# Kernel optimization log

Measured on AMD Instinct MI355X. Metric: run time of the kernel, lower is better.

The kernel has to match this reference:

```python
import jax, jax.numpy as jnp
import numpy as np

B, S, H = 2, 2048, 1024
NH, HD = 16, 64            # num heads, head dim
R = 8                      # lora rank
LORA_SCALE = 64.0 / 8.0    # lora_alpha / lora_rank
SCALE = jnp.sqrt(jnp.float32(HD))


def setup_inputs() -> dict:
    key = jax.random.key(0)
    ks = jax.random.split(key, 14)
    std = 1.0 / np.sqrt(H)
    p = {
        'hidden_states': jax.random.normal(ks[0], (B, S, H), jnp.float32),
        'attention_mask': jnp.ones((B, S), jnp.float32),
        # base projections, stored [in, out] so y = x @ W
        'Wq': jax.random.normal(ks[1], (H, H), jnp.float32) * std,
        'Wk': jax.random.normal(ks[2], (H, H), jnp.float32) * std,
        'Wv': jax.random.normal(ks[3], (H, H), jnp.float32) * std,
        'Wo': jax.random.normal(ks[4], (H, H), jnp.float32) * std,
        # LoRA down (A: [H,R]) / up (B: [R,H]) for q,k,v,output
        'Aq': jax.random.normal(ks[5], (H, R), jnp.float32) * 0.01,
        'Bq': jax.random.normal(ks[6], (R, H), jnp.float32) * 0.01,
        'Ak': jax.random.normal(ks[7], (H, R), jnp.float32) * 0.01,
        'Bk': jax.random.normal(ks[8], (R, H), jnp.float32) * 0.01,
        'Av': jax.random.normal(ks[9], (H, R), jnp.float32) * 0.01,
        'Bv': jax.random.normal(ks[10], (R, H), jnp.float32) * 0.01,
        'Ao': jax.random.normal(ks[11], (H, R), jnp.float32) * 0.01,
        'Bo': jax.random.normal(ks[12], (R, H), jnp.float32) * 0.01,
    }
    return p


def _heads(x):
    # [B,S,H] -> [B,NH,S,HD]
    return x.reshape(B, S, NH, HD).transpose(0, 2, 1, 3)


def reference(hidden_states, attention_mask, Wq, Wk, Wv, Wo,
              Aq, Bq, Ak, Bk, Av, Bv, Ao, Bo):
    hs = hidden_states
    sg = jax.lax.stop_gradient  # freeze_base=True: base projections are no_grad

    q = sg(hs @ Wq) + (hs @ Aq) @ Bq * LORA_SCALE
    k = sg(hs @ Wk) + (hs @ Ak) @ Bk * LORA_SCALE
    v = sg(hs @ Wv) + (hs @ Av) @ Bv * LORA_SCALE

    qh, kh, vh = _heads(q), _heads(k), _heads(v)  # [B,NH,S,HD]

    scores = jnp.einsum('bhqd,bhkd->bhqk', qh, kh) / SCALE  # [B,NH,S,S]
    mask = (1.0 - attention_mask)[:, None, None, :] * -10000.0
    scores = scores + mask
    probs = jax.nn.softmax(scores, axis=-1)  # dropout is identity in eval

    ctx = jnp.einsum('bhqk,bhkd->bhqd', probs, vh)
    ctx = ctx.transpose(0, 2, 1, 3).reshape(B, S, H)

    out = sg(ctx @ Wo) + (ctx @ Ao) @ Bo * LORA_SCALE
    return out
```

## Files before the change

### kernel.cpp

```cpp
#include <hip/hip_runtime.h>
#include <math.h>

typedef float fx4 __attribute__((ext_vector_type(4)));
typedef float f32x4 __attribute__((ext_vector_type(4)));
typedef short bf16x8 __attribute__((ext_vector_type(8)));
typedef unsigned short us4 __attribute__((ext_vector_type(4)));
typedef unsigned short us8 __attribute__((ext_vector_type(8)));
typedef unsigned int u32x4 __attribute__((ext_vector_type(4)));

#define HDIM 1024
#define SEQ  2048
#define BATCH 2
#define NHEAD 16
#define HD    64
#define MTOT  4096
#define LSCALE 8.0f
#define LOG2E 1.44269504088896340736f

__device__ __forceinline__ unsigned short f2bf(float f) {
    union { float f; unsigned int u; } v; v.f = f;
    unsigned int r = v.u + 0x7FFFu + ((v.u >> 16) & 1u);
    return (unsigned short)(r >> 16);
}
__device__ __forceinline__ float bf2f(unsigned short h) {
    union { unsigned int u; float f; } v; v.u = ((unsigned int)h) << 16;
    return v.f;
}
__device__ __forceinline__ unsigned int cvt_pk_bf16(float a, float b) {
    unsigned int r;
    asm("v_cvt_pk_bf16_f32 %0, %1, %2" : "=v"(r) : "v"(a), "v"(b));
    return r;
}

__global__ __launch_bounds__(256)
void split_x_kernel(const float* __restrict__ X, unsigned short* __restrict__ Xh,
                    unsigned short* __restrict__ Xl, int n4)
{
    int i = blockIdx.x * 256 + threadIdx.x;
    int stride = gridDim.x * 256;
    for (; i < n4; i += stride) {
        fx4 v = *((const fx4*)X + i);
        us4 h, l;
#pragma unroll
        for (int j = 0; j < 4; ++j) {
            h[j] = f2bf(v[j]);
            l[j] = f2bf(v[j] - bf2f(h[j]));
        }
        *((us4*)Xh + i) = h;
        *((us4*)Xl + i) = l;
    }
}

__global__ __launch_bounds__(256)
void tsplit_w_kernel(const float* __restrict__ W0, const float* __restrict__ W1,
                     const float* __restrict__ W2, const float* __restrict__ W3,
                     unsigned short* __restrict__ WTbase)
{
    int z = blockIdx.z;
    const float* W = (z == 0) ? W0 : (z == 1) ? W1 : (z == 2) ? W2 : W3;
    unsigned short* WTh = WTbase + (size_t)z * 2097152;
    unsigned short* WTl = WTh + 1048576;
    int n0 = blockIdx.x * 64, k0 = blockIdx.y * 64;
    __shared__ unsigned int T[64][65];
    int t = threadIdx.x;
#pragma unroll
    for (int i = 0; i < 4; ++i) {
        int idx = t + 256 * i;
        int r = idx >> 4, c4 = (idx & 15) * 4;
        fx4 w = *(const fx4*)&W[(size_t)(k0 + r) * HDIM + n0 + c4];
#pragma unroll
        for (int j = 0; j < 4; ++j) {
            unsigned short hi = f2bf(w[j]);
            unsigned short lo = f2bf(w[j] - bf2f(hi));
            T[r][c4 + j] = (unsigned int)hi | ((unsigned int)lo << 16);
        }
    }
    __syncthreads();
#pragma unroll
    for (int i = 0; i < 4; ++i) {
        int idx = t + 256 * i;
        int n = idx >> 4, kg = (idx & 15) * 4;
        us4 hv, lv;
#pragma unroll
        for (int j = 0; j < 4; ++j) {
            unsigned int p = T[kg + j][n];
            hv[j] = (unsigned short)(p & 0xffffu);
            lv[j] = (unsigned short)(p >> 16);
        }
        *(us4*)&WTh[(size_t)(n0 + n) * HDIM + k0 + kg] = hv;
        *(us4*)&WTl[(size_t)(n0 + n) * HDIM + k0 + kg] = lv;
    }
}

__global__ __launch_bounds__(256)
void transpose_v_kernel(const unsigned short* __restrict__ vb,
                        unsigned short* __restrict__ vt)
{
    int s0 = blockIdx.x * 64;
    int bh = blockIdx.y;
    int b = bh >> 4, h = bh & 15;
    __shared__ unsigned short T[64][80];
    int t = threadIdx.x;
#pragma unroll
    for (int i = 0; i < 2; ++i) {
        int u = t + 256 * i;
        int r = u >> 3, cg = u & 7;
        us8 v = *(const us8*)&vb[(size_t)(b * SEQ + s0 + r) * HDIM + h * HD + 8 * cg];
        *(us8*)&T[r][8 * cg] = v;
    }
    __syncthreads();
#pragma unroll
    for (int i = 0; i < 2; ++i) {
        int u = t + 256 * i;
        int d = u & 63, sg = u >> 6;
        us8 v;
#pragma unroll
        for (int j = 0; j < 8; ++j) v[j] = T[8 * sg + j][d];
        *(us8*)&vt[(size_t)(bh * HD + d) * SEQ + s0 + 8 * sg] = v;
    }
}

__global__ __launch_bounds__(64)
void lora_down_kernel(const float* __restrict__ X,
                      const float* __restrict__ A0,
                      const float* __restrict__ A1,
                      const float* __restrict__ A2,
                      float* __restrict__ out, int nmat)
{
    int row  = blockIdx.x;
    int lane = threadIdx.x;
    const float* xr = X + (size_t)row * HDIM;
    float xv[16];
#pragma unroll
    for (int i = 0; i < 16; ++i) xv[i] = xr[lane + 64 * i];
    const float* Amats[3] = {A0, A1, A2};
    for (int m = 0; m < nmat; ++m) {
        const float* A = Amats[m];
        float s[8];
#pragma unroll
        for (int c = 0; c < 8; ++c) s[c] = 0.f;
#pragma unroll
        for (int i = 0; i < 16; ++i) {
            const float* ap = A + (size_t)(lane + 64 * i) * 8;
#pragma unroll
            for (int c = 0; c < 8; ++c) s[c] += xv[i] * ap[c];
        }
#pragma unroll
        for (int c = 0; c < 8; ++c) {
#pragma unroll
            for (int off = 1; off < 64; off <<= 1)
                s[c] += __shfl_xor(s[c], off, 64);
        }
        if (lane == 0) {
#pragma unroll
            for (int c = 0; c < 8; ++c)
                out[(size_t)row * 24 + m * 8 + c] = s[c];
        }
    }
}

__global__ __launch_bounds__(64)
void lora_down_bf_kernel(const unsigned short* __restrict__ Xh,
                         const unsigned short* __restrict__ Xl,
                         const float* __restrict__ A,
                         float* __restrict__ out)
{
    int row  = blockIdx.x;
    int lane = threadIdx.x;
    const unsigned short* xh = Xh + (size_t)row * HDIM;
    const unsigned short* xl = Xl + (size_t)row * HDIM;
    float xv[16];
#pragma unroll
    for (int i = 0; i < 16; ++i)
        xv[i] = bf2f(xh[lane + 64 * i]) + bf2f(xl[lane + 64 * i]);
    float s[8];
#pragma unroll
    for (int c = 0; c < 8; ++c) s[c] = 0.f;
#pragma unroll
    for (int i = 0; i < 16; ++i) {
        const float* ap = A + (size_t)(lane + 64 * i) * 8;
#pragma unroll
        for (int c = 0; c < 8; ++c) s[c] += xv[i] * ap[c];
    }
#pragma unroll
    for (int c = 0; c < 8; ++c) {
#pragma unroll
        for (int off = 1; off < 64; off <<= 1)
            s[c] += __shfl_xor(s[c], off, 64);
    }
    if (lane == 0) {
#pragma unroll
        for (int c = 0; c < 8; ++c) out[(size_t)row * 8 + c] = s[c];
    }
}

template<bool OUTF32, int BM>
__global__ __launch_bounds__(256, BM == 128 ? 2 : 3)
void gemm_mfma_kernel(const unsigned short* __restrict__ Xh, const unsigned short* __restrict__ Xl,
                      const unsigned short* __restrict__ WTbase, int wsel0,
                      const float* __restrict__ XA, int xa_stride, int xa_off0,
                      const float* __restrict__ Bu0, const float* __restrict__ Bu1, const float* __restrict__ Bu2,
                      void* __restrict__ O0, void* __restrict__ O1, void* __restrict__ O2)
{
    constexpr int FN = (BM == 128) ? 4 : 2;
    int pz = blockIdx.z;
    const unsigned short* WTh = WTbase + (size_t)(wsel0 + pz) * 2097152;
    const unsigned short* WTl = WTh + 1048576;
    const float* Bu = (pz == 0) ? Bu0 : (pz == 1) ? Bu1 : Bu2;
    void* Ovp       = (pz == 0) ? O0 : (pz == 1) ? O1 : O2;
    int xa_off = xa_off0 + pz * 8;

    int brow = blockIdx.y * BM, bcol = blockIdx.x * 128;
    int t = threadIdx.x, wid = t >> 6, lane = t & 63, l15 = lane & 15, g = lane >> 4;
    int wm = (BM == 128) ? (wid >> 1) * 64 : 0;
    int wn = (BM == 128) ? (wid & 1) * 64 : wid * 32;

    __shared__ unsigned short Ah[BM][40];
    __shared__ unsigned short Al[BM][40];
    __shared__ unsigned short Bh[128][40];
    __shared__ unsigned short Bl[128][40];

    f32x4 acc[4][FN];
#pragma unroll
    for (int i = 0; i < 4; ++i)
#pragma unroll
        for (int j = 0; j < FN; ++j) acc[i][j] = (f32x4){0.f, 0.f, 0.f, 0.f};

    int sm = t >> 2, skg = t & 3;
    const unsigned short* aH0 = Xh  + (size_t)(brow + sm) * HDIM + 8 * skg;
    const unsigned short* aL0 = Xl  + (size_t)(brow + sm) * HDIM + 8 * skg;
    const unsigned short* bH0 = WTh + (size_t)(bcol + sm) * HDIM + 8 * skg;
    const unsigned short* bL0 = WTl + (size_t)(bcol + sm) * HDIM + 8 * skg;
    const size_t R64 = (size_t)64 * HDIM;

    us8 rAH0, rAH1, rAL0, rAL1, rBH0, rBH1, rBL0, rBL1;
    rAH0 = *(const us8*)(aH0);
    rAL0 = *(const us8*)(aL0);
    if (BM == 128) {
        rAH1 = *(const us8*)(aH0 + R64);
        rAL1 = *(const us8*)(aL0 + R64);
    }
    rBH0 = *(const us8*)(bH0);
    rBH1 = *(const us8*)(bH0 + R64);
    rBL0 = *(const us8*)(bL0);
    rBL1 = *(const us8*)(bL0 + R64);

    for (int k0 = 0; k0 < HDIM; k0 += 32) {
        __syncthreads();
        *(us8*)&Ah[sm][8 * skg] = rAH0;
        *(us8*)&Al[sm][8 * skg] = rAL0;
        if (BM == 128) {
            *(us8*)&Ah[(sm + 64) & (BM - 1)][8 * skg] = rAH1;
            *(us8*)&Al[(sm + 64) & (BM - 1)][8 * skg] = rAL1;
        }
        *(us8*)&Bh[sm][8 * skg]      = rBH0;
        *(us8*)&Bh[sm + 64][8 * skg] = rBH1;
        *(us8*)&Bl[sm][8 * skg]      = rBL0;
        *(us8*)&Bl[sm + 64][8 * skg] = rBL1;
        __syncthreads();
        if (k0 + 32 < HDIM) {
            int ko = k0 + 32;
            rAH0 = *(const us8*)(aH0 + ko);
            rAL0 = *(const us8*)(aL0 + ko);
            if (BM == 128) {
                rAH1 = *(const us8*)(aH0 + R64 + ko);
                rAL1 = *(const us8*)(aL0 + R64 + ko);
            }
            rBH0 = *(const us8*)(bH0 + ko);
            rBH1 = *(const us8*)(bH0 + R64 + ko);
            rBL0 = *(const us8*)(bL0 + ko);
            rBL1 = *(const us8*)(bL0 + R64 + ko);
        }
        bf16x8 fah[4], fal[4], fbh[FN], fbl[FN];
#pragma unroll
        for (int f = 0; f < 4; ++f) {
            fah[f] = *(const bf16x8*)&Ah[wm + 16 * f + l15][8 * g];
            fal[f] = *(const bf16x8*)&Al[wm + 16 * f + l15][8 * g];
        }
#pragma unroll
        for (int f = 0; f < FN; ++f) {
            fbh[f] = *(const bf16x8*)&Bh[wn + 16 * f + l15][8 * g];
            fbl[f] = *(const bf16x8*)&Bl[wn + 16 * f + l15][8 * g];
        }
#pragma unroll
        for (int fm = 0; fm < 4; ++fm)
#pragma unroll
            for (int fn = 0; fn < FN; ++fn) {
                f32x4 a = acc[fm][fn];
                a = __builtin_amdgcn_mfma_f32_16x16x32_bf16(fah[fm], fbh[fn], a, 0, 0, 0);
                a = __builtin_amdgcn_mfma_f32_16x16x32_bf16(fah[fm], fbl[fn], a, 0, 0, 0);
                a = __builtin_amdgcn_mfma_f32_16x16x32_bf16(fal[fm], fbh[fn], a, 0, 0, 0);
                acc[fm][fn] = a;
            }
    }

    float lb[8][FN];
#pragma unroll
    for (int rr = 0; rr < 8; ++rr)
#pragma unroll
        for (int fn = 0; fn < FN; ++fn)
            lb[rr][fn] = Bu[(size_t)rr * HDIM + bcol + wn + 16 * fn + l15] * LSCALE;

#pragma unroll
    for (int fm = 0; fm < 4; ++fm) {
        float la[4][8];
#pragma unroll
        for (int r = 0; r < 4; ++r) {
            int row = brow + wm + 16 * fm + 4 * g + r;
            const float* lap = XA + (size_t)row * xa_stride + xa_off;
            fx4 q0 = *(const fx4*)lap;
            fx4 q1 = *(const fx4*)(lap + 4);
#pragma unroll
            for (int j = 0; j < 4; ++j) { la[r][j] = q0[j]; la[r][4 + j] = q1[j]; }
        }
#pragma unroll
        for (int fn = 0; fn < FN; ++fn)
#pragma unroll
            for (int r = 0; r < 4; ++r) {
                float sum = acc[fm][fn][r];
#pragma unroll
                for (int rr = 0; rr < 8; ++rr) sum += la[r][rr] * lb[rr][fn];
                size_t row = (size_t)(brow + wm + 16 * fm + 4 * g + r);
                int col = bcol + wn + 16 * fn + l15;
                if (OUTF32) ((float*)Ovp)[row * HDIM + col] = sum;
                else ((unsigned short*)Ovp)[row * HDIM + col] = f2bf(sum);
            }
    }
}

#define QBLK 64
#define KVB  64
#define NT   (SEQ / KVB)

__global__ __launch_bounds__(256, 4)
void attn_mfma_kernel(const unsigned short* __restrict__ Qg, const unsigned short* __restrict__ Kg,
                      const unsigned short* __restrict__ Vt, const float* __restrict__ mask,
                      unsigned short* __restrict__ Ch, unsigned short* __restrict__ Cl)
{
    int qt = blockIdx.x, h = blockIdx.y, b = blockIdx.z;
    int t    = threadIdx.x;
    int wid  = t >> 6;
    int lane = t & 63;
    int l15  = lane & 15;
    int g    = lane >> 4;

    __shared__ __align__(16) unsigned short Ks[2][64][72];
    __shared__ __align__(16) unsigned short Vs[2][64][72];
    __shared__ __align__(16) float Msd[2][64];

    bf16x8 qa[2];
    const unsigned short* qp = Qg + (size_t)(b * SEQ + qt * QBLK + wid * 16) * HDIM + h * HD;
#pragma unroll
    for (int kc = 0; kc < 2; ++kc)
        qa[kc] = *(const bf16x8*)(qp + (size_t)l15 * HDIM + 32 * kc + 8 * g);

    float m0 = 0.f;
    f32x4 l4 = (f32x4){0.f, 0.f, 0.f, 0.f};
    f32x4 acc[4];
#pragma unroll
    for (int n = 0; n < 4; ++n) acc[n] = (f32x4){0.f, 0.f, 0.f, 0.f};

    const unsigned short* kp0 = Kg + (size_t)(b * SEQ) * HDIM + h * HD;
    const unsigned short* vt0 = Vt + (size_t)((b * NHEAD + h) * HD) * SEQ;

    const float QSCL = 0.125f * LOG2E;
    const float MSCL = -10000.0f * LOG2E;

    int r0 = t >> 3,           c0 = (t & 7) * 8;
    int r1 = (t + 256) >> 3,   c1 = c0;

    *(us8*)&Ks[0][r0][c0] = *(const us8*)(kp0 + (size_t)r0 * HDIM + c0);
    *(us8*)&Ks[0][r1][c1] = *(const us8*)(kp0 + (size_t)r1 * HDIM + c1);
    *(us8*)&Vs[0][r0][c0] = *(const us8*)(vt0 + (size_t)r0 * SEQ + c0);
    *(us8*)&Vs[0][r1][c1] = *(const us8*)(vt0 + (size_t)r1 * SEQ + c1);
    if (t < 64) Msd[0][t] = (1.0f - mask[b * SEQ + t]) * MSCL;
    __syncthreads();

    int cur = 0;
    for (int kt = 0; kt < NT; ++kt) {
        us8 knr0, knr1, vnr0, vnr1;
        float mreg = 1.0f;
        bool more = (kt + 1 < NT);
        if (more) {
            const unsigned short* kp = kp0 + (size_t)(kt + 1) * KVB * HDIM;
            const unsigned short* vp = vt0 + (kt + 1) * KVB;
            knr0 = *(const us8*)(kp + (size_t)r0 * HDIM + c0);
            knr1 = *(const us8*)(kp + (size_t)r1 * HDIM + c1);
            vnr0 = *(const us8*)(vp + (size_t)r0 * SEQ + c0);
            vnr1 = *(const us8*)(vp + (size_t)r1 * SEQ + c1);
            if (t < 64) mreg = mask[b * SEQ + (kt + 1) * KVB + t];
        }

        f32x4 sT[4];
#pragma unroll
        for (int n = 0; n < 4; ++n) {
            f32x4 a = (f32x4){0.f, 0.f, 0.f, 0.f};
#pragma unroll
            for (int kc = 0; kc < 2; ++kc) {
                bf16x8 kb = *(const bf16x8*)&Ks[cur][16 * n + l15][32 * kc + 8 * g];
                a = __builtin_amdgcn_mfma_f32_16x16x32_bf16(kb, qa[kc], a, 0, 0, 0);
            }
            sT[n] = a;
        }

#pragma unroll
        for (int n = 0; n < 4; ++n) {
            fx4 msk = *(const fx4*)&Msd[cur][16 * n + 4 * g];
#pragma unroll
            for (int r = 0; r < 4; ++r) sT[n][r] = fmaf(sT[n][r], QSCL, msk[r]);
        }

        if (kt == 0) {
            f32x4 t01, t23, tt;
#pragma unroll
            for (int r = 0; r < 4; ++r) {
                t01[r] = fmaxf(sT[0][r], sT[1][r]);
                t23[r] = fmaxf(sT[2][r], sT[3][r]);
                tt[r]  = fmaxf(t01[r], t23[r]);
            }
            float mx = fmaxf(fmaxf(tt[0], tt[1]), fmaxf(tt[2], tt[3]));
            mx = fmaxf(mx, __shfl_xor(mx, 16, 64));
            mx = fmaxf(mx, __shfl_xor(mx, 32, 64));
            m0 = fmaxf(mx, -64.f);
        }

#pragma unroll
        for (int n = 0; n < 4; ++n)
#pragma unroll
            for (int r = 0; r < 4; ++r) {
                float p = exp2f(sT[n][r] - m0);
                sT[n][r] = p;
                l4[r] += p;
            }

        unsigned int pkx[4], pky[4];
#pragma unroll
        for (int n = 0; n < 4; ++n) {
            pkx[n] = cvt_pk_bf16(sT[n][0], sT[n][1]);
            pky[n] = cvt_pk_bf16(sT[n][2], sT[n][3]);
        }

        int lA = l15 + 32 * (g & 1);
        int lB = lA + 16;
        bool selhi = (g & 2) != 0;
        bf16x8 pb[2];
#pragma unroll
        for (int kc = 0; kc < 2; ++kc) {
            unsigned int xA0 = __shfl((int)pkx[2 * kc], lA, 64);
            unsigned int yA0 = __shfl((int)pky[2 * kc], lA, 64);
            unsigned int xA1 = __shfl((int)pkx[2 * kc + 1], lA, 64);
            unsigned int yA1 = __shfl((int)pky[2 * kc + 1], lA, 64);
            unsigned int xB0 = __shfl((int)pkx[2 * kc], lB, 64);
            unsigned int yB0 = __shfl((int)pky[2 * kc], lB, 64);
            unsigned int xB1 = __shfl((int)pkx[2 * kc + 1], lB, 64);
            unsigned int yB1 = __shfl((int)pky[2 * kc + 1], lB, 64);
            u32x4 d;
            d[0] = selhi ? xA1 : xA0;
            d[1] = selhi ? yA1 : yA0;
            d[2] = selhi ? xB1 : xB0;
            d[3] = selhi ? yB1 : yB0;
            pb[kc] = *(bf16x8*)&d;
        }

#pragma unroll
        for (int n = 0; n < 4; ++n)
#pragma unroll
            for (int kc = 0; kc < 2; ++kc) {
                bf16x8 vb = *(const bf16x8*)&Vs[cur][16 * n + l15][32 * kc + 8 * g];
                acc[n] = __builtin_amdgcn_mfma_f32_16x16x32_bf16(vb, pb[kc], acc[n], 0, 0, 0);
            }

        if (more) {
            *(us8*)&Ks[cur ^ 1][r0][c0] = knr0;
            *(us8*)&Ks[cur ^ 1][r1][c1] = knr1;
            *(us8*)&Vs[cur ^ 1][r0][c0] = vnr0;
            *(us8*)&Vs[cur ^ 1][r1][c1] = vnr1;
            if (t < 64) Msd[cur ^ 1][t] = (1.0f - mreg) * MSCL;
        }
        __syncthreads();
        cur ^= 1;
    }

    float l = (l4[0] + l4[1]) + (l4[2] + l4[3]);
    l += __shfl_xor(l, 16, 64);
    l += __shfl_xor(l, 32, 64);
    float inv = 1.0f / l;
    size_t row = (size_t)(b * SEQ + qt * QBLK + wid * 16 + l15);
#pragma unroll
    for (int n = 0; n < 4; ++n) {
        us4 hv, lv;
#pragma unroll
        for (int r = 0; r < 4; ++r) {
            float o = acc[n][r] * inv;
            unsigned short hi = f2bf(o);
            hv[r] = hi;
            lv[r] = f2bf(o - bf2f(hi));
        }
        size_t idx = row * HDIM + h * HD + 16 * n + 4 * g;
        *(us4*)&Ch[idx] = hv;
        *(us4*)&Cl[idx] = lv;
    }
}

extern "C" void kernel_launch(void* const* d_in, const int* in_sizes, int n_in,
                              void* d_out, int out_size, void* d_ws, size_t ws_size,
                              hipStream_t stream)
{
    const float* hs   = (const float*)d_in[0];
    const float* mask = (const float*)d_in[1];
    const float* Wq = (const float*)d_in[2];
    const float* Wk = (const float*)d_in[3];
    const float* Wv = (const float*)d_in[4];
    const float* Wo = (const float*)d_in[5];
    const float* Aq = (const float*)d_in[6];
    const float* Bq = (const float*)d_in[7];
    const float* Ak = (const float*)d_in[8];
    const float* Bk = (const float*)d_in[9];
    const float* Av = (const float*)d_in[10];
    const float* Bv = (const float*)d_in[11];
    const float* Ao = (const float*)d_in[12];
    const float* Bo = (const float*)d_in[13];
    float* out = (float*)d_out;

    char* w = (char*)d_ws;
    unsigned short* Xh = (unsigned short*)(w);
    unsigned short* Xl = (unsigned short*)(w + ((size_t)8 << 20));
    unsigned short* WT = (unsigned short*)(w + ((size_t)16 << 20));
    unsigned short* qb = (unsigned short*)(w + ((size_t)32 << 20));
    unsigned short* kb = (unsigned short*)(w + ((size_t)40 << 20));
    unsigned short* vb = (unsigned short*)(w + ((size_t)48 << 20));
    unsigned short* vt = (unsigned short*)(w + ((size_t)56 << 20));
    float* hsA  = (float*)(w + ((size_t)64 << 20));
    float* ctxA = (float*)(w + ((size_t)64 << 20) + 400 * 1024);

    split_x_kernel<<<2048, 256, 0, stream>>>(hs, Xh, Xl, MTOT * HDIM / 4);
    tsplit_w_kernel<<<dim3(16, 16, 4), 256, 0, stream>>>(Wq, Wk, Wv, Wo, WT);
    lora_down_kernel<<<MTOT, 64, 0, stream>>>(hs, Aq, Ak, Av, hsA, 3);
    gemm_mfma_kernel<false, 128><<<dim3(8, 32, 3), 256, 0, stream>>>(
        Xh, Xl, WT, 0, hsA, 24, 0, Bq, Bk, Bv, qb, kb, vb);
    transpose_v_kernel<<<dim3(SEQ / 64, BATCH * NHEAD), 256, 0, stream>>>(vb, vt);
    attn_mfma_kernel<<<dim3(SEQ / QBLK, NHEAD, BATCH), 256, 0, stream>>>(
        qb, kb, vt, mask, Xh , Xl );
    lora_down_bf_kernel<<<MTOT, 64, 0, stream>>>(Xh, Xl, Ao, ctxA);
    gemm_mfma_kernel<true, 64><<<dim3(8, 64, 1), 256, 0, stream>>>(
        Xh, Xl, WT, 3, ctxA, 8, 0, Bo, Bo, Bo, out, out, out);
}
```

Before: 245.4 us.

## Process two query subtiles per wave in attention to reuse K/V fragments

Doubles the query block to 128 rows, with each wave computing two 16-row subtiles against the same K and V LDS fragments. This halves LDS reads and global K/V loads per query and gives more independent MFMAs per loaded fragment. In exchange it uses more registers, lowers the launch-bounds occupancy target and halves the number of blocks, which reduces parallelism and latency hiding.

After: 240.1 us. -2.2%, faster.

```diff
diff --git a/kernel.cpp b/kernel.cpp
--- a/kernel.cpp
+++ b/kernel.cpp
@@ -328,11 +328,11 @@
     }
 }
 
-#define QBLK 64
+#define QBLK 128
 #define KVB  64
 #define NT   (SEQ / KVB)
 
-__global__ __launch_bounds__(256, 4)
+__global__ __launch_bounds__(256, 2)
 void attn_mfma_kernel(const unsigned short* __restrict__ Qg, const unsigned short* __restrict__ Kg,
                       const unsigned short* __restrict__ Vt, const float* __restrict__ mask,
                       unsigned short* __restrict__ Ch, unsigned short* __restrict__ Cl)
@@ -348,17 +348,23 @@
     __shared__ __align__(16) unsigned short Vs[2][64][72];
     __shared__ __align__(16) float Msd[2][64];
 
-    bf16x8 qa[2];
-    const unsigned short* qp = Qg + (size_t)(b * SEQ + qt * QBLK + wid * 16) * HDIM + h * HD;
-#pragma unroll
-    for (int kc = 0; kc < 2; ++kc)
-        qa[kc] = *(const bf16x8*)(qp + (size_t)l15 * HDIM + 32 * kc + 8 * g);
-
-    float m0 = 0.f;
-    f32x4 l4 = (f32x4){0.f, 0.f, 0.f, 0.f};
-    f32x4 acc[4];
-#pragma unroll
-    for (int n = 0; n < 4; ++n) acc[n] = (f32x4){0.f, 0.f, 0.f, 0.f};
+    bf16x8 qa[2][2];
+    const unsigned short* qp = Qg + (size_t)(b * SEQ + qt * QBLK + wid * 32) * HDIM + h * HD;
+#pragma unroll
+    for (int m = 0; m < 2; ++m)
+#pragma unroll
+        for (int kc = 0; kc < 2; ++kc)
+            qa[m][kc] = *(const bf16x8*)(qp + (size_t)(16 * m + l15) * HDIM + 32 * kc + 8 * g);
+
+    float m0[2] = {0.f, 0.f};
+    f32x4 l4[2];
+    f32x4 acc[2][4];
+#pragma unroll
+    for (int m = 0; m < 2; ++m) {
+        l4[m] = (f32x4){0.f, 0.f, 0.f, 0.f};
+#pragma unroll
+        for (int n = 0; n < 4; ++n) acc[m][n] = (f32x4){0.f, 0.f, 0.f, 0.f};
+    }
 
     const unsigned short* kp0 = Kg + (size_t)(b * SEQ) * HDIM + h * HD;
     const unsigned short* vt0 = Vt + (size_t)((b * NHEAD + h) * HD) * SEQ;
@@ -391,84 +397,97 @@
             if (t < 64) mreg = mask[b * SEQ + (kt + 1) * KVB + t];
         }
 
-        f32x4 sT[4];
+        f32x4 sT[2][4];
 #pragma unroll
         for (int n = 0; n < 4; ++n) {
-            f32x4 a = (f32x4){0.f, 0.f, 0.f, 0.f};
-#pragma unroll
-            for (int kc = 0; kc < 2; ++kc) {
-                bf16x8 kb = *(const bf16x8*)&Ks[cur][16 * n + l15][32 * kc + 8 * g];
-                a = __builtin_amdgcn_mfma_f32_16x16x32_bf16(kb, qa[kc], a, 0, 0, 0);
-            }
-            sT[n] = a;
+            bf16x8 kb0 = *(const bf16x8*)&Ks[cur][16 * n + l15][8 * g];
+            bf16x8 kb1 = *(const bf16x8*)&Ks[cur][16 * n + l15][32 + 8 * g];
+#pragma unroll
+            for (int m = 0; m < 2; ++m) {
+                f32x4 a = (f32x4){0.f, 0.f, 0.f, 0.f};
+                a = __builtin_amdgcn_mfma_f32_16x16x32_bf16(kb0, qa[m][0], a, 0, 0, 0);
+                a = __builtin_amdgcn_mfma_f32_16x16x32_bf16(kb1, qa[m][1], a, 0, 0, 0);
+                sT[m][n] = a;
+            }
         }
 
 #pragma unroll
         for (int n = 0; n < 4; ++n) {
             fx4 msk = *(const fx4*)&Msd[cur][16 * n + 4 * g];
 #pragma unroll
-            for (int r = 0; r < 4; ++r) sT[n][r] = fmaf(sT[n][r], QSCL, msk[r]);
+            for (int m = 0; m < 2; ++m)
+#pragma unroll
+                for (int r = 0; r < 4; ++r) sT[m][n][r] = fmaf(sT[m][n][r], QSCL, msk[r]);
         }
 
         if (kt == 0) {
-            f32x4 t01, t23, tt;
-#pragma unroll
-            for (int r = 0; r < 4; ++r) {
-                t01[r] = fmaxf(sT[0][r], sT[1][r]);
-                t23[r] = fmaxf(sT[2][r], sT[3][r]);
-                tt[r]  = fmaxf(t01[r], t23[r]);
-            }
-            float mx = fmaxf(fmaxf(tt[0], tt[1]), fmaxf(tt[2], tt[3]));
-            mx = fmaxf(mx, __shfl_xor(mx, 16, 64));
-            mx = fmaxf(mx, __shfl_xor(mx, 32, 64));
-            m0 = fmaxf(mx, -64.f);
-        }
-
-#pragma unroll
-        for (int n = 0; n < 4; ++n)
-#pragma unroll
-            for (int r = 0; r < 4; ++r) {
-                float p = exp2f(sT[n][r] - m0);
-                sT[n][r] = p;
-                l4[r] += p;
-            }
-
-        unsigned int pkx[4], pky[4];
-#pragma unroll
-        for (int n = 0; n < 4; ++n) {
-            pkx[n] = cvt_pk_bf16(sT[n][0], sT[n][1]);
-            pky[n] = cvt_pk_bf16(sT[n][2], sT[n][3]);
-        }
+#pragma unroll
+            for (int m = 0; m < 2; ++m) {
+                f32x4 tt;
+#pragma unroll
+                for (int r = 0; r < 4; ++r)
+                    tt[r] = fmaxf(fmaxf(sT[m][0][r], sT[m][1][r]), fmaxf(sT[m][2][r], sT[m][3][r]));
+                float mx = fmaxf(fmaxf(tt[0], tt[1]), fmaxf(tt[2], tt[3]));
+                mx = fmaxf(mx, __shfl_xor(mx, 16, 64));
+                mx = fmaxf(mx, __shfl_xor(mx, 32, 64));
+                m0[m] = fmaxf(mx, -64.f);
+            }
+        }
+
+#pragma unroll
+        for (int m = 0; m < 2; ++m)
+#pragma unroll
+            for (int n = 0; n < 4; ++n)
+#pragma unroll
+                for (int r = 0; r < 4; ++r) {
+                    float p = exp2f(sT[m][n][r] - m0[m]);
+                    sT[m][n][r] = p;
+                    l4[m][r] += p;
+                }
 
         int lA = l15 + 32 * (g & 1);
         int lB = lA + 16;
         bool selhi = (g & 2) != 0;
-        bf16x8 pb[2];
-#pragma unroll
-        for (int kc = 0; kc < 2; ++kc) {
-            unsigned int xA0 = __shfl((int)pkx[2 * kc], lA, 64);
-            unsigned int yA0 = __shfl((int)pky[2 * kc], lA, 64);
-            unsigned int xA1 = __shfl((int)pkx[2 * kc + 1], lA, 64);
-            unsigned int yA1 = __shfl((int)pky[2 * kc + 1], lA, 64);
-            unsigned int xB0 = __shfl((int)pkx[2 * kc], lB, 64);
-            unsigned int yB0 = __shfl((int)pky[2 * kc], lB, 64);
-            unsigned int xB1 = __shfl((int)pkx[2 * kc + 1], lB, 64);
-            unsigned int yB1 = __shfl((int)pky[2 * kc + 1], lB, 64);
-            u32x4 d;
-            d[0] = selhi ? xA1 : xA0;
-            d[1] = selhi ? yA1 : yA0;
-            d[2] = selhi ? xB1 : xB0;
-            d[3] = selhi ? yB1 : yB0;
-            pb[kc] = *(bf16x8*)&d;
-        }
-
-#pragma unroll
-        for (int n = 0; n < 4; ++n)
+        bf16x8 pb[2][2];
+#pragma unroll
+        for (int m = 0; m < 2; ++m) {
+            unsigned int pkx[4], pky[4];
+#pragma unroll
+            for (int n = 0; n < 4; ++n) {
+                pkx[n] = cvt_pk_bf16(sT[m][n][0], sT[m][n][1]);
+                pky[n] = cvt_pk_bf16(sT[m][n][2], sT[m][n][3]);
+            }
 #pragma unroll
             for (int kc = 0; kc < 2; ++kc) {
-                bf16x8 vb = *(const bf16x8*)&Vs[cur][16 * n + l15][32 * kc + 8 * g];
-                acc[n] = __builtin_amdgcn_mfma_f32_16x16x32_bf16(vb, pb[kc], acc[n], 0, 0, 0);
-            }
+                unsigned int xA0 = __shfl((int)pkx[2 * kc], lA, 64);
+                unsigned int yA0 = __shfl((int)pky[2 * kc], lA, 64);
+                unsigned int xA1 = __shfl((int)pkx[2 * kc + 1], lA, 64);
+                unsigned int yA1 = __shfl((int)pky[2 * kc + 1], lA, 64);
+                unsigned int xB0 = __shfl((int)pkx[2 * kc], lB, 64);
+                unsigned int yB0 = __shfl((int)pky[2 * kc], lB, 64);
+                unsigned int xB1 = __shfl((int)pkx[2 * kc + 1], lB, 64);
+                unsigned int yB1 = __shfl((int)pky[2 * kc + 1], lB, 64);
+                u32x4 d;
+                d[0] = selhi ? xA1 : xA0;
+                d[1] = selhi ? yA1 : yA0;
+                d[2] = selhi ? xB1 : xB0;
+                d[3] = selhi ? yB1 : yB0;
+                pb[m][kc] = *(bf16x8*)&d;
+            }
+        }
+
+#pragma unroll
+        for (int n = 0; n < 4; ++n) {
+            bf16x8 vb0 = *(const bf16x8*)&Vs[cur][16 * n + l15][8 * g];
+            bf16x8 vb1 = *(const bf16x8*)&Vs[cur][16 * n + l15][32 + 8 * g];
+#pragma unroll
+            for (int m = 0; m < 2; ++m) {
+                f32x4 a = acc[m][n];
+                a = __builtin_amdgcn_mfma_f32_16x16x32_bf16(vb0, pb[m][0], a, 0, 0, 0);
+                a = __builtin_amdgcn_mfma_f32_16x16x32_bf16(vb1, pb[m][1], a, 0, 0, 0);
+                acc[m][n] = a;
+            }
+        }
 
         if (more) {
             *(us8*)&Ks[cur ^ 1][r0][c0] = knr0;
@@ -481,24 +500,27 @@
         cur ^= 1;
     }
 
-    float l = (l4[0] + l4[1]) + (l4[2] + l4[3]);
-    l += __shfl_xor(l, 16, 64);
-    l += __shfl_xor(l, 32, 64);
-    float inv = 1.0f / l;
-    size_t row = (size_t)(b * SEQ + qt * QBLK + wid * 16 + l15);
-#pragma unroll
-    for (int n = 0; n < 4; ++n) {
-        us4 hv, lv;
-#pragma unroll
-        for (int r = 0; r < 4; ++r) {
-            float o = acc[n][r] * inv;
-            unsigned short hi = f2bf(o);
-            hv[r] = hi;
-            lv[r] = f2bf(o - bf2f(hi));
-        }
-        size_t idx = row * HDIM + h * HD + 16 * n + 4 * g;
-        *(us4*)&Ch[idx] = hv;
-        *(us4*)&Cl[idx] = lv;
+#pragma unroll
+    for (int m = 0; m < 2; ++m) {
+        float l = (l4[m][0] + l4[m][1]) + (l4[m][2] + l4[m][3]);
+        l += __shfl_xor(l, 16, 64);
+        l += __shfl_xor(l, 32, 64);
+        float inv = 1.0f / l;
+        size_t row = (size_t)(b * SEQ + qt * QBLK + wid * 32 + 16 * m + l15);
+#pragma unroll
+        for (int n = 0; n < 4; ++n) {
+            us4 hv, lv;
+#pragma unroll
+            for (int r = 0; r < 4; ++r) {
+                float o = acc[m][n][r] * inv;
+                unsigned short hi = f2bf(o);
+                hv[r] = hi;
+                lv[r] = f2bf(o - bf2f(hi));
+            }
+            size_t idx = row * HDIM + h * HD + 16 * n + 4 * g;
+            *(us4*)&Ch[idx] = hv;
+            *(us4*)&Cl[idx] = lv;
+        }
     }
 }
 
```

## Switch attention to 32x32 MFMA with 128-row Q tiles; fuse V transpose into GEMM epilogue

Applied to the files above, without the earlier changes.

The attention kernel now processes 128 query rows per block, with each wave owning 32 rows. It uses 32x32x16 bf16 MFMAs in place of 16x16x32 and repacks P with v_permlane32_swap instead of eight shuffles. The QKV GEMM epilogue writes V straight into the transposed head-major layout, so the separate transpose_v kernel and the round trip through the vb buffer are removed. The aim is fewer shuffles, better reuse of LDS K/V tiles per block, and one fewer launch. The costs are occupancy halved to 2 blocks per CU and half as many attention blocks, plus scattered 8-byte stores in the V epilogue.

New measurement: 228.5 us. 6.9% less time.

```diff
diff --git a/kernel.cpp b/kernel.cpp
--- a/kernel.cpp
+++ b/kernel.cpp
@@ -3,6 +3,7 @@
 
 typedef float fx4 __attribute__((ext_vector_type(4)));
 typedef float f32x4 __attribute__((ext_vector_type(4)));
+typedef float f32x16 __attribute__((ext_vector_type(16)));
 typedef short bf16x8 __attribute__((ext_vector_type(8)));
 typedef unsigned short us4 __attribute__((ext_vector_type(4)));
 typedef unsigned short us8 __attribute__((ext_vector_type(8)));
@@ -92,34 +93,6 @@
     }
 }
 
-__global__ __launch_bounds__(256)
-void transpose_v_kernel(const unsigned short* __restrict__ vb,
-                        unsigned short* __restrict__ vt)
-{
-    int s0 = blockIdx.x * 64;
-    int bh = blockIdx.y;
-    int b = bh >> 4, h = bh & 15;
-    __shared__ unsigned short T[64][80];
-    int t = threadIdx.x;
-#pragma unroll
-    for (int i = 0; i < 2; ++i) {
-        int u = t + 256 * i;
-        int r = u >> 3, cg = u & 7;
-        us8 v = *(const us8*)&vb[(size_t)(b * SEQ + s0 + r) * HDIM + h * HD + 8 * cg];
-        *(us8*)&T[r][8 * cg] = v;
-    }
-    __syncthreads();
-#pragma unroll
-    for (int i = 0; i < 2; ++i) {
-        int u = t + 256 * i;
-        int d = u & 63, sg = u >> 6;
-        us8 v;
-#pragma unroll
-        for (int j = 0; j < 8; ++j) v[j] = T[8 * sg + j][d];
-        *(us8*)&vt[(size_t)(bh * HD + d) * SEQ + s0 + 8 * sg] = v;
-    }
-}
-
 __global__ __launch_bounds__(64)
 void lora_down_kernel(const float* __restrict__ X,
                       const float* __restrict__ A0,
@@ -200,7 +173,8 @@
                       const unsigned short* __restrict__ WTbase, int wsel0,
                       const float* __restrict__ XA, int xa_stride, int xa_off0,
                       const float* __restrict__ Bu0, const float* __restrict__ Bu1, const float* __restrict__ Bu2,
-                      void* __restrict__ O0, void* __restrict__ O1, void* __restrict__ O2)
+                      void* __restrict__ O0, void* __restrict__ O1, void* __restrict__ O2,
+                      int vtpz, unsigned short* __restrict__ vtout)
 {
     constexpr int FN = (BM == 128) ? 4 : 2;
     int pz = blockIdx.z;
@@ -314,54 +288,73 @@
             for (int j = 0; j < 4; ++j) { la[r][j] = q0[j]; la[r][4 + j] = q1[j]; }
         }
 #pragma unroll
-        for (int fn = 0; fn < FN; ++fn)
+        for (int fn = 0; fn < FN; ++fn) {
+            float tmp[4];
 #pragma unroll
             for (int r = 0; r < 4; ++r) {
                 float sum = acc[fm][fn][r];
 #pragma unroll
                 for (int rr = 0; rr < 8; ++rr) sum += la[r][rr] * lb[rr][fn];
-                size_t row = (size_t)(brow + wm + 16 * fm + 4 * g + r);
-                int col = bcol + wn + 16 * fn + l15;
-                if (OUTF32) ((float*)Ovp)[row * HDIM + col] = sum;
-                else ((unsigned short*)Ovp)[row * HDIM + col] = f2bf(sum);
-            }
-    }
-}
-
-#define QBLK 64
+                tmp[r] = sum;
+            }
+            int col  = bcol + wn + 16 * fn + l15;
+            int rowb = brow + wm + 16 * fm + 4 * g;
+            if (pz == vtpz) {
+                int hh = col >> 6, d = col & 63;
+                int bb = rowb >> 11, ss = rowb & 2047;
+                us4 hv;
+#pragma unroll
+                for (int r = 0; r < 4; ++r) hv[r] = f2bf(tmp[r]);
+                *(us4*)&vtout[(size_t)((bb * NHEAD + hh) * HD + d) * SEQ + ss] = hv;
+            } else if (OUTF32) {
+#pragma unroll
+                for (int r = 0; r < 4; ++r)
+                    ((float*)Ovp)[(size_t)(rowb + r) * HDIM + col] = tmp[r];
+            } else {
+#pragma unroll
+                for (int r = 0; r < 4; ++r)
+                    ((unsigned short*)Ovp)[(size_t)(rowb + r) * HDIM + col] = f2bf(tmp[r]);
+            }
+        }
+    }
+}
+
+#define QBLK 128
 #define KVB  64
 #define NT   (SEQ / KVB)
 
-__global__ __launch_bounds__(256, 4)
+__global__ __launch_bounds__(256, 2)
 void attn_mfma_kernel(const unsigned short* __restrict__ Qg, const unsigned short* __restrict__ Kg,
                       const unsigned short* __restrict__ Vt, const float* __restrict__ mask,
                       unsigned short* __restrict__ Ch, unsigned short* __restrict__ Cl)
 {
-    int qt = blockIdx.x, h = blockIdx.y, b = blockIdx.z;
+    int qt = blockIdx.x, hd = blockIdx.y, b = blockIdx.z;
     int t    = threadIdx.x;
     int wid  = t >> 6;
     int lane = t & 63;
-    int l15  = lane & 15;
-    int g    = lane >> 4;
+    int q31  = lane & 31;
+    int g1   = lane >> 5;
 
     __shared__ __align__(16) unsigned short Ks[2][64][72];
     __shared__ __align__(16) unsigned short Vs[2][64][72];
     __shared__ __align__(16) float Msd[2][64];
 
-    bf16x8 qa[2];
-    const unsigned short* qp = Qg + (size_t)(b * SEQ + qt * QBLK + wid * 16) * HDIM + h * HD;
-#pragma unroll
-    for (int kc = 0; kc < 2; ++kc)
-        qa[kc] = *(const bf16x8*)(qp + (size_t)l15 * HDIM + 32 * kc + 8 * g);
+    bf16x8 qB[4];
+    const unsigned short* qp = Qg + (size_t)(b * SEQ + qt * QBLK + wid * 32 + q31) * HDIM + hd * HD;
+#pragma unroll
+    for (int kc = 0; kc < 4; ++kc)
+        qB[kc] = *(const bf16x8*)(qp + 16 * kc + 8 * g1);
 
     float m0 = 0.f;
     f32x4 l4 = (f32x4){0.f, 0.f, 0.f, 0.f};
-    f32x4 acc[4];
-#pragma unroll
-    for (int n = 0; n < 4; ++n) acc[n] = (f32x4){0.f, 0.f, 0.f, 0.f};
-
-    const unsigned short* kp0 = Kg + (size_t)(b * SEQ) * HDIM + h * HD;
-    const unsigned short* vt0 = Vt + (size_t)((b * NHEAD + h) * HD) * SEQ;
+    f32x16 accO[2];
+#pragma unroll
+    for (int dh = 0; dh < 2; ++dh)
+#pragma unroll
+        for (int i = 0; i < 16; ++i) accO[dh][i] = 0.f;
+
+    const unsigned short* kp0 = Kg + (size_t)(b * SEQ) * HDIM + hd * HD;
+    const unsigned short* vt0 = Vt + (size_t)((b * NHEAD + hd) * HD) * SEQ;
 
     const float QSCL = 0.125f * LOG2E;
     const float MSCL = -10000.0f * LOG2E;
@@ -391,84 +384,84 @@
             if (t < 64) mreg = mask[b * SEQ + (kt + 1) * KVB + t];
         }
 
-        f32x4 sT[4];
-#pragma unroll
-        for (int n = 0; n < 4; ++n) {
-            f32x4 a = (f32x4){0.f, 0.f, 0.f, 0.f};
-#pragma unroll
-            for (int kc = 0; kc < 2; ++kc) {
-                bf16x8 kb = *(const bf16x8*)&Ks[cur][16 * n + l15][32 * kc + 8 * g];
-                a = __builtin_amdgcn_mfma_f32_16x16x32_bf16(kb, qa[kc], a, 0, 0, 0);
-            }
-            sT[n] = a;
-        }
-
-#pragma unroll
-        for (int n = 0; n < 4; ++n) {
-            fx4 msk = *(const fx4*)&Msd[cur][16 * n + 4 * g];
-#pragma unroll
-            for (int r = 0; r < 4; ++r) sT[n][r] = fmaf(sT[n][r], QSCL, msk[r]);
-        }
+        f32x16 sQ[2];
+#pragma unroll
+        for (int kvh = 0; kvh < 2; ++kvh) {
+            f32x16 a;
+#pragma unroll
+            for (int i = 0; i < 16; ++i) a[i] = 0.f;
+#pragma unroll
+            for (int kc = 0; kc < 4; ++kc) {
+                bf16x8 kA = *(const bf16x8*)&Ks[cur][32 * kvh + q31][16 * kc + 8 * g1];
+                a = __builtin_amdgcn_mfma_f32_32x32x16_bf16(kA, qB[kc], a, 0, 0, 0);
+            }
+            sQ[kvh] = a;
+        }
+
+#pragma unroll
+        for (int kvh = 0; kvh < 2; ++kvh)
+#pragma unroll
+            for (int hh = 0; hh < 4; ++hh) {
+                fx4 msk = *(const fx4*)&Msd[cur][32 * kvh + 8 * hh + 4 * g1];
+#pragma unroll
+                for (int r = 0; r < 4; ++r)
+                    sQ[kvh][4 * hh + r] = fmaf(sQ[kvh][4 * hh + r], QSCL, msk[r]);
+            }
 
         if (kt == 0) {
-            f32x4 t01, t23, tt;
-#pragma unroll
-            for (int r = 0; r < 4; ++r) {
-                t01[r] = fmaxf(sT[0][r], sT[1][r]);
-                t23[r] = fmaxf(sT[2][r], sT[3][r]);
-                tt[r]  = fmaxf(t01[r], t23[r]);
-            }
-            float mx = fmaxf(fmaxf(tt[0], tt[1]), fmaxf(tt[2], tt[3]));
-            mx = fmaxf(mx, __shfl_xor(mx, 16, 64));
+            float mx = sQ[0][0];
+#pragma unroll
+            for (int kvh = 0; kvh < 2; ++kvh)
+#pragma unroll
+                for (int i = 0; i < 16; ++i) mx = fmaxf(mx, sQ[kvh][i]);
             mx = fmaxf(mx, __shfl_xor(mx, 32, 64));
             m0 = fmaxf(mx, -64.f);
         }
 
 #pragma unroll
-        for (int n = 0; n < 4; ++n)
-#pragma unroll
-            for (int r = 0; r < 4; ++r) {
-                float p = exp2f(sT[n][r] - m0);
-                sT[n][r] = p;
-                l4[r] += p;
-            }
-
-        unsigned int pkx[4], pky[4];
-#pragma unroll
-        for (int n = 0; n < 4; ++n) {
-            pkx[n] = cvt_pk_bf16(sT[n][0], sT[n][1]);
-            pky[n] = cvt_pk_bf16(sT[n][2], sT[n][3]);
-        }
-
-        int lA = l15 + 32 * (g & 1);
-        int lB = lA + 16;
-        bool selhi = (g & 2) != 0;
-        bf16x8 pb[2];
-#pragma unroll
-        for (int kc = 0; kc < 2; ++kc) {
-            unsigned int xA0 = __shfl((int)pkx[2 * kc], lA, 64);
-            unsigned int yA0 = __shfl((int)pky[2 * kc], lA, 64);
-            unsigned int xA1 = __shfl((int)pkx[2 * kc + 1], lA, 64);
-            unsigned int yA1 = __shfl((int)pky[2 * kc + 1], lA, 64);
-            unsigned int xB0 = __shfl((int)pkx[2 * kc], lB, 64);
-            unsigned int yB0 = __shfl((int)pky[2 * kc], lB, 64);
-            unsigned int xB1 = __shfl((int)pkx[2 * kc + 1], lB, 64);
-            unsigned int yB1 = __shfl((int)pky[2 * kc + 1], lB, 64);
-            u32x4 d;
-            d[0] = selhi ? xA1 : xA0;
-            d[1] = selhi ? yA1 : yA0;
-            d[2] = selhi ? xB1 : xB0;
-            d[3] = selhi ? yB1 : yB0;
-            pb[kc] = *(bf16x8*)&d;
-        }
-
-#pragma unroll
-        for (int n = 0; n < 4; ++n)
-#pragma unroll
-            for (int kc = 0; kc < 2; ++kc) {
-                bf16x8 vb = *(const bf16x8*)&Vs[cur][16 * n + l15][32 * kc + 8 * g];
-                acc[n] = __builtin_amdgcn_mfma_f32_16x16x32_bf16(vb, pb[kc], acc[n], 0, 0, 0);
-            }
+        for (int kvh = 0; kvh < 2; ++kvh)
+#pragma unroll
+            for (int hh = 0; hh < 4; ++hh)
+#pragma unroll
+                for (int r = 0; r < 4; ++r) {
+                    float p = exp2f(sQ[kvh][4 * hh + r] - m0);
+                    sQ[kvh][4 * hh + r] = p;
+                    l4[r] += p;
+                }
+
+        unsigned int pkx[2][4], pky[2][4];
+#pragma unroll
+        for (int kvh = 0; kvh < 2; ++kvh)
+#pragma unroll
+            for (int hh = 0; hh < 4; ++hh) {
+                pkx[kvh][hh] = cvt_pk_bf16(sQ[kvh][4 * hh + 0], sQ[kvh][4 * hh + 1]);
+                pky[kvh][hh] = cvt_pk_bf16(sQ[kvh][4 * hh + 2], sQ[kvh][4 * hh + 3]);
+            }
+
+        bf16x8 pB[4];
+#pragma unroll
+        for (int kvh = 0; kvh < 2; ++kvh)
+#pragma unroll
+            for (int kc2 = 0; kc2 < 2; ++kc2) {
+                unsigned int x0 = pkx[kvh][2 * kc2], x1 = pkx[kvh][2 * kc2 + 1];
+                unsigned int y0 = pky[kvh][2 * kc2], y1 = pky[kvh][2 * kc2 + 1];
+                asm("v_permlane32_swap_b32 %0, %1" : "+v"(x0), "+v"(x1));
+                asm("v_permlane32_swap_b32 %0, %1" : "+v"(y0), "+v"(y1));
+                u32x4 dd;
+                dd[0] = x0; dd[1] = y0; dd[2] = x1; dd[3] = y1;
+                pB[2 * kvh + kc2] = *(bf16x8*)&dd;
+            }
+
+#pragma unroll
+        for (int dh = 0; dh < 2; ++dh) {
+            f32x16 a = accO[dh];
+#pragma unroll
+            for (int kcp = 0; kcp < 4; ++kcp) {
+                bf16x8 vA = *(const bf16x8*)&Vs[cur][32 * dh + q31][16 * kcp + 8 * g1];
+                a = __builtin_amdgcn_mfma_f32_32x32x16_bf16(vA, pB[kcp], a, 0, 0, 0);
+            }
+            accO[dh] = a;
+        }
 
         if (more) {
             *(us8*)&Ks[cur ^ 1][r0][c0] = knr0;
@@ -482,24 +475,25 @@
     }
 
     float l = (l4[0] + l4[1]) + (l4[2] + l4[3]);
-    l += __shfl_xor(l, 16, 64);
     l += __shfl_xor(l, 32, 64);
     float inv = 1.0f / l;
-    size_t row = (size_t)(b * SEQ + qt * QBLK + wid * 16 + l15);
-#pragma unroll
-    for (int n = 0; n < 4; ++n) {
-        us4 hv, lv;
-#pragma unroll
-        for (int r = 0; r < 4; ++r) {
-            float o = acc[n][r] * inv;
-            unsigned short hi = f2bf(o);
-            hv[r] = hi;
-            lv[r] = f2bf(o - bf2f(hi));
-        }
-        size_t idx = row * HDIM + h * HD + 16 * n + 4 * g;
-        *(us4*)&Ch[idx] = hv;
-        *(us4*)&Cl[idx] = lv;
-    }
+    size_t row = (size_t)(b * SEQ + qt * QBLK + wid * 32 + q31);
+#pragma unroll
+    for (int dh = 0; dh < 2; ++dh)
+#pragma unroll
+        for (int hh = 0; hh < 4; ++hh) {
+            us4 hv, lv;
+#pragma unroll
+            for (int r = 0; r < 4; ++r) {
+                float o = accO[dh][4 * hh + r] * inv;
+                unsigned short hi = f2bf(o);
+                hv[r] = hi;
+                lv[r] = f2bf(o - bf2f(hi));
+            }
+            size_t idx = row * HDIM + hd * HD + 32 * dh + 8 * hh + 4 * g1;
+            *(us4*)&Ch[idx] = hv;
+            *(us4*)&Cl[idx] = lv;
+        }
 }
 
 extern "C" void kernel_launch(void* const* d_in, const int* in_sizes, int n_in,
@@ -528,7 +522,6 @@
     unsigned short* WT = (unsigned short*)(w + ((size_t)16 << 20));
     unsigned short* qb = (unsigned short*)(w + ((size_t)32 << 20));
     unsigned short* kb = (unsigned short*)(w + ((size_t)40 << 20));
-    unsigned short* vb = (unsigned short*)(w + ((size_t)48 << 20));
     unsigned short* vt = (unsigned short*)(w + ((size_t)56 << 20));
     float* hsA  = (float*)(w + ((size_t)64 << 20));
     float* ctxA = (float*)(w + ((size_t)64 << 20) + 400 * 1024);
@@ -537,11 +530,10 @@
     tsplit_w_kernel<<<dim3(16, 16, 4), 256, 0, stream>>>(Wq, Wk, Wv, Wo, WT);
     lora_down_kernel<<<MTOT, 64, 0, stream>>>(hs, Aq, Ak, Av, hsA, 3);
     gemm_mfma_kernel<false, 128><<<dim3(8, 32, 3), 256, 0, stream>>>(
-        Xh, Xl, WT, 0, hsA, 24, 0, Bq, Bk, Bv, qb, kb, vb);
-    transpose_v_kernel<<<dim3(SEQ / 64, BATCH * NHEAD), 256, 0, stream>>>(vb, vt);
+        Xh, Xl, WT, 0, hsA, 24, 0, Bq, Bk, Bv, qb, kb, nullptr, 2, vt);
     attn_mfma_kernel<<<dim3(SEQ / QBLK, NHEAD, BATCH), 256, 0, stream>>>(
         qb, kb, vt, mask, Xh , Xl );
     lora_down_bf_kernel<<<MTOT, 64, 0, stream>>>(Xh, Xl, Ao, ctxA);
     gemm_mfma_kernel<true, 64><<<dim3(8, 64, 1), 256, 0, stream>>>(
-        Xh, Xl, WT, 3, ctxA, 8, 0, Bo, Bo, Bo, out, out, out);
-}
+        Xh, Xl, WT, 3, ctxA, 8, 0, Bo, Bo, Bo, out, out, out, -1, nullptr);
+}
```
